# Performance work log

Hardware: AMD Instinct MI355X
Metric: run time of the kernel (lower is better)

The kernel has to match this reference:

```python
import jax, jax.numpy as jnp
import numpy as np

B, S, H = 1, 2048, 1024      # batch, seq, hidden_size
F = 4096                     # intermediate_size
E = 8                        # num_experts
K = 2                        # top-k routing


def setup_inputs() -> dict:
    key = jax.random.key(0)
    ks = jax.random.split(key, 7)
    s = 0.02  # init scale
    return {
        "x": jax.random.normal(ks[0], (B, S, H), jnp.float32),
        "gate_w": jax.random.normal(ks[1], (H, E), jnp.float32) * s,
        "gate_b": jnp.zeros((E,), jnp.float32),
        "w1": jax.random.normal(ks[2], (E, H, F), jnp.float32) * s,
        "b1": jnp.zeros((E, F), jnp.float32),
        "w2": jax.random.normal(ks[3], (E, F, H), jnp.float32) * s,
        "b2": jnp.zeros((E, H), jnp.float32),
    }


def reference(x, gate_w, gate_b, w1, b1, w2, b2):
    Bq, Sq, Hq = x.shape
    T = Bq * Sq
    xt = x.reshape(T, Hq)                              # [T,H] flatten tokens

    # --- router: softmax gate, top-k, renormalize top-k weights ---
    logits = xt @ gate_w + gate_b                      # [T,E]
    probs = jax.nn.softmax(logits, axis=-1)            # [T,E]
    top_v, top_i = jax.lax.top_k(probs, K)             # [T,K]
    top_v = top_v / jnp.sum(top_v, axis=-1, keepdims=True)
    combine = jnp.zeros((T, E), x.dtype).at[jnp.arange(T)[:, None], top_i].set(top_v)  # [T,E] sparse combine weights

    # --- experts: 2-layer FFN (ReLU), batched over experts ---
    h = jax.nn.relu(jnp.einsum('th,ehf->etf', xt, w1) + b1[:, None, :])   # [E,T,F]
    y = jnp.einsum('etf,efh->eth', h, w2) + b2[:, None, :]                # [E,T,H]

    # --- combine: weighted sum over selected experts (zeros elsewhere) ---
    out = jnp.einsum('te,eth->th', combine, y)          # [T,H]
    return out.reshape(Bq, Sq, Hq)
```

## Files before the change

kernel.cpp:

```cpp
#include <hip/hip_runtime.h>

#define TT 2048
#define HH 1024
#define FF 4096
#define EE 8
#define ROWS_CAP 5120
#define KSPLIT2 4

typedef __bf16 bf16;
typedef bf16 bf16x8 __attribute__((ext_vector_type(8)));
typedef bf16 bf16x4 __attribute__((ext_vector_type(4)));
typedef bf16 bf16x2 __attribute__((ext_vector_type(2)));
typedef float floatx4 __attribute__((ext_vector_type(4)));

#define OFF_W1T  ((size_t)0)
#define OFF_W2T  (OFF_W1T + (size_t)67108864)
#define OFF_XG   (OFF_W2T + (size_t)67108864)
#define OFF_H    (OFF_XG  + (size_t)10485760)
#define OFF_CNT  (OFF_H   + (size_t)41943040)
#define OFF_OFS  (OFF_CNT + (size_t)256)
#define OFF_TKE  (OFF_OFS + (size_t)256)
#define OFF_TKR  (OFF_TKE + (size_t)16384)
#define OFF_TKW  (OFF_TKR + (size_t)16384)
#define OFF_ROW  (OFF_TKW + (size_t)16384)
#define OFF_Y    OFF_W1T

__device__ __forceinline__ void gload16(const bf16* g, bf16* l) {
    __builtin_amdgcn_global_load_lds((const __attribute__((address_space(1))) void*)g,
                                     (__attribute__((address_space(3))) void*)l, 16, 0, 0);
}

__global__ __launch_bounds__(256) void transpose_cvt(const float* __restrict__ in,
                                                     bf16* __restrict__ out,
                                                     int R, int C) {
    __shared__ float tile[64][67];
    const int e  = blockIdx.z;
    const int r0 = blockIdx.y * 64, c0 = blockIdx.x * 64;
    const float* inp = in + (size_t)e * R * C;
    bf16* outp = out + (size_t)e * R * C;
    const int t = threadIdx.x;
    {
        const int lr = t >> 4;
        const int lc = (t & 15) << 2;
#pragma unroll
        for (int i = 0; i < 4; ++i) {
            int r = lr + i * 16;
            floatx4 v = *(const floatx4*)&inp[(size_t)(r0 + r) * C + c0 + lc];
            tile[r][lc + 0] = v[0]; tile[r][lc + 1] = v[1];
            tile[r][lc + 2] = v[2]; tile[r][lc + 3] = v[3];
        }
    }
    __syncthreads();
    {
        const int c  = t >> 3;
        const int rq = (t & 7) << 3;
#pragma unroll
        for (int i = 0; i < 2; ++i) {
            int cc = c + i * 32;
            bf16x8 o;
#pragma unroll
            for (int k = 0; k < 8; ++k) o[k] = (bf16)tile[rq + k][cc];
            *(bf16x8*)&outp[(size_t)(c0 + cc) * R + r0 + rq] = o;
        }
    }
}

__global__ __launch_bounds__(256) void router_kernel(const float* __restrict__ x,
                                                     const float* __restrict__ gw,
                                                     const float* __restrict__ gb,
                                                     int* __restrict__ counts,
                                                     int* __restrict__ tke,
                                                     int* __restrict__ tkr,
                                                     float* __restrict__ tkw) {
    const int wave = blockIdx.x * 4 + (threadIdx.x >> 6);
    const int lane = threadIdx.x & 63;
    const int nw = gridDim.x * 4;
    for (int t = wave; t < TT; t += nw) {
        const float* xr = x + (size_t)t * HH;
        double acc[EE];
#pragma unroll
        for (int e = 0; e < EE; ++e) acc[e] = 0.0;
        for (int h = lane; h < HH; h += 64) {
            double xv = (double)xr[h];
            const float* g = gw + (size_t)h * EE;
            floatx4 g0 = *(const floatx4*)&g[0];
            floatx4 g1 = *(const floatx4*)&g[4];
            acc[0] += xv * (double)g0[0]; acc[1] += xv * (double)g0[1];
            acc[2] += xv * (double)g0[2]; acc[3] += xv * (double)g0[3];
            acc[4] += xv * (double)g1[0]; acc[5] += xv * (double)g1[1];
            acc[6] += xv * (double)g1[2]; acc[7] += xv * (double)g1[3];
        }
#pragma unroll
        for (int e = 0; e < EE; ++e) {
            double v = acc[e];
            for (int s = 32; s > 0; s >>= 1) v += __shfl_xor(v, s, 64);
            acc[e] = v + (double)gb[e];
        }
        if (lane == 0) {
            int i1 = 0; double v1 = acc[0];
            for (int e = 1; e < EE; ++e) if (acc[e] > v1) { v1 = acc[e]; i1 = e; }
            int i2 = -1; double v2 = -1e300;
            for (int e = 0; e < EE; ++e) if (e != i1 && acc[e] > v2) { v2 = acc[e]; i2 = e; }
            double wa = 1.0 / (1.0 + exp(v2 - v1));
            double wb = 1.0 - wa;
            int r1 = atomicAdd(&counts[i1], 1);
            int r2 = atomicAdd(&counts[i2], 1);
            tke[t * 2 + 0] = i1; tke[t * 2 + 1] = i2;
            tkr[t * 2 + 0] = r1; tkr[t * 2 + 1] = r2;
            tkw[t * 2 + 0] = (float)wa; tkw[t * 2 + 1] = (float)wb;
        }
    }
}

__global__ void scan_offsets(const int* __restrict__ counts, int* __restrict__ offs) {
    if (threadIdx.x == 0 && blockIdx.x == 0) {
        int off = 0;
        for (int e = 0; e < EE; ++e) {
            offs[e] = off;
            off += (counts[e] + 127) & ~127;
        }
    }
}

__global__ __launch_bounds__(256) void gather_kernel(const float* __restrict__ x,
                                                     const int* __restrict__ tke,
                                                     const int* __restrict__ tkr,
                                                     const int* __restrict__ offs,
                                                     bf16* __restrict__ xg,
                                                     int* __restrict__ rowOf) {
    const int pair = blockIdx.x;
    const int t = pair >> 1;
    const int e = tke[pair];
    const int row = offs[e] + tkr[pair];
    const float* xr = x + (size_t)t * HH;
    bf16* dst = xg + (size_t)row * HH;
    const int tid = threadIdx.x;
    floatx4 v = ((const floatx4*)xr)[tid];
    bf16x4 o;
    o[0] = (bf16)v[0]; o[1] = (bf16)v[1]; o[2] = (bf16)v[2]; o[3] = (bf16)v[3];
    ((bf16x4*)dst)[tid] = o;
    if (tid == 0) rowOf[pair] = row;
}

__global__ __launch_bounds__(256, 2) void gemm1_kernel(const bf16* __restrict__ A,
                                                       const bf16* __restrict__ Bt,
                                                       const float* __restrict__ b1,
                                                       bf16* __restrict__ Hout,
                                                       const int* __restrict__ counts,
                                                       const int* __restrict__ offs) {
    const int e = blockIdx.z, mt = blockIdx.y, nt = blockIdx.x;
    const int cnt = counts[e];
    if (mt * 128 >= cnt) return;
    const int row0 = offs[e] + mt * 128;
    const int K = HH;
    const bf16* Ab = A + (size_t)row0 * K;
    const bf16* Bb = Bt + ((size_t)e * FF + (size_t)nt * 128) * K;

    __shared__ bf16 As[128 * 32];
    __shared__ bf16 Bs[128 * 32];

    const int tid = threadIdx.x;
    const int lane = tid & 63, wave = tid >> 6;
    const int lrow = lane & 15, lq = lane >> 4;
    const int m_w = (wave & 1) << 6, n_w = (wave >> 1) << 6;
    const int swz = (lrow >> 1) & 3;
    const unsigned foff = (unsigned)((lq ^ swz) << 3);

    floatx4 acc[4][4];
#pragma unroll
    for (int i = 0; i < 4; ++i)
#pragma unroll
        for (int j = 0; j < 4; ++j) acc[i][j] = (floatx4){0.f, 0.f, 0.f, 0.f};

    const int c0 = tid, c1 = tid + 256;
    const int ar0 = c0 >> 2, ak0 = (c0 & 3) ^ ((ar0 >> 1) & 3);
    const int ar1 = c1 >> 2, ak1 = (c1 & 3) ^ ((ar1 >> 1) & 3);
    const unsigned lds0 = (unsigned)((tid & ~63) << 4);
    const unsigned lds1 = 4096u + lds0;
    const size_t ga0 = (size_t)ar0 * K + ak0 * 8;
    const size_t ga1 = (size_t)ar1 * K + ak1 * 8;

    for (int kt = 0; kt < K / 32; ++kt) {
        const int kb = kt * 32;
        gload16(Ab + ga0 + kb, (bf16*)((char*)As + lds0));
        gload16(Ab + ga1 + kb, (bf16*)((char*)As + lds1));
        gload16(Bb + ga0 + kb, (bf16*)((char*)Bs + lds0));
        gload16(Bb + ga1 + kb, (bf16*)((char*)Bs + lds1));
        asm volatile("s_waitcnt vmcnt(0)" ::: "memory");
        __syncthreads();

        bf16x8 af[4], bfr[4];
#pragma unroll
        for (int i = 0; i < 4; ++i) {
            int m = m_w + i * 16 + lrow;
            af[i] = *(const bf16x8*)&As[(unsigned)m * 32 + foff];
        }
#pragma unroll
        for (int j = 0; j < 4; ++j) {
            int n = n_w + j * 16 + lrow;
            bfr[j] = *(const bf16x8*)&Bs[(unsigned)n * 32 + foff];
        }
#pragma unroll
        for (int i = 0; i < 4; ++i)
#pragma unroll
            for (int j = 0; j < 4; ++j)
                acc[i][j] = __builtin_amdgcn_mfma_f32_16x16x32_bf16(af[i], bfr[j], acc[i][j], 0, 0, 0);
        __syncthreads();
    }

    const float* bias = b1 + (size_t)e * FF + (size_t)nt * 128;
    bf16* Hb = Hout + (size_t)row0 * FF + (size_t)nt * 128;
#pragma unroll
    for (int j = 0; j < 4; ++j) {
        int col = n_w + j * 16 + lrow;
        float bv = bias[col];
#pragma unroll
        for (int i = 0; i < 4; ++i)
#pragma unroll
            for (int r = 0; r < 4; ++r) {
                int mrow = m_w + i * 16 + (lq << 2) + r;
                float v = acc[i][j][r] + bv;
                Hb[(size_t)mrow * FF + col] = (bf16)(v > 0.f ? v : 0.f);
            }
    }
}

__global__ __launch_bounds__(256, 2) void gemm2_kernel(const bf16* __restrict__ Hin,
                                                       const bf16* __restrict__ Bt,
                                                       const float* __restrict__ b2,
                                                       bf16* __restrict__ Y,
                                                       const int* __restrict__ counts,
                                                       const int* __restrict__ offs) {
    const int e = blockIdx.z >> 2, ks = blockIdx.z & 3;
    const int mt = blockIdx.y, nt = blockIdx.x;
    const int cnt = counts[e];
    if (mt * 128 >= cnt) return;
    const int row0 = offs[e] + mt * 128;
    const int K = FF;
    const int KC = FF / KSPLIT2;
    const bf16* Ab = Hin + (size_t)row0 * K + ks * KC;
    const bf16* Bb = Bt + ((size_t)e * HH + (size_t)nt * 128) * K + ks * KC;

    __shared__ bf16 As[128 * 32];
    __shared__ bf16 Bs[128 * 32];

    const int tid = threadIdx.x;
    const int lane = tid & 63, wave = tid >> 6;
    const int lrow = lane & 15, lq = lane >> 4;
    const int m_w = (wave & 1) << 6, n_w = (wave >> 1) << 6;
    const int swz = (lrow >> 1) & 3;
    const unsigned foff = (unsigned)((lq ^ swz) << 3);

    floatx4 acc[4][4];
#pragma unroll
    for (int i = 0; i < 4; ++i)
#pragma unroll
        for (int j = 0; j < 4; ++j) acc[i][j] = (floatx4){0.f, 0.f, 0.f, 0.f};

    const int c0 = tid, c1 = tid + 256;
    const int ar0 = c0 >> 2, ak0 = (c0 & 3) ^ ((ar0 >> 1) & 3);
    const int ar1 = c1 >> 2, ak1 = (c1 & 3) ^ ((ar1 >> 1) & 3);
    const unsigned lds0 = (unsigned)((tid & ~63) << 4);
    const unsigned lds1 = 4096u + lds0;
    const size_t ga0 = (size_t)ar0 * K + ak0 * 8;
    const size_t ga1 = (size_t)ar1 * K + ak1 * 8;

    for (int kt = 0; kt < KC / 32; ++kt) {
        const int kb = kt * 32;
        gload16(Ab + ga0 + kb, (bf16*)((char*)As + lds0));
        gload16(Ab + ga1 + kb, (bf16*)((char*)As + lds1));
        gload16(Bb + ga0 + kb, (bf16*)((char*)Bs + lds0));
        gload16(Bb + ga1 + kb, (bf16*)((char*)Bs + lds1));
        asm volatile("s_waitcnt vmcnt(0)" ::: "memory");
        __syncthreads();

        bf16x8 af[4], bfr[4];
#pragma unroll
        for (int i = 0; i < 4; ++i) {
            int m = m_w + i * 16 + lrow;
            af[i] = *(const bf16x8*)&As[(unsigned)m * 32 + foff];
        }
#pragma unroll
        for (int j = 0; j < 4; ++j) {
            int n = n_w + j * 16 + lrow;
            bfr[j] = *(const bf16x8*)&Bs[(unsigned)n * 32 + foff];
        }
#pragma unroll
        for (int i = 0; i < 4; ++i)
#pragma unroll
            for (int j = 0; j < 4; ++j)
                acc[i][j] = __builtin_amdgcn_mfma_f32_16x16x32_bf16(af[i], bfr[j], acc[i][j], 0, 0, 0);
        __syncthreads();
    }

    const float* bias = b2 + (size_t)e * HH + (size_t)nt * 128;
    bf16* Yb = Y + ((size_t)ks * ROWS_CAP + row0) * HH + (size_t)nt * 128;
#pragma unroll
    for (int j = 0; j < 4; ++j) {
        int col = n_w + j * 16 + lrow;
        float bv = (ks == 0) ? bias[col] : 0.f;
#pragma unroll
        for (int i = 0; i < 4; ++i)
#pragma unroll
            for (int r = 0; r < 4; ++r) {
                int mrow = m_w + i * 16 + (lq << 2) + r;
                Yb[(size_t)mrow * HH + col] = (bf16)(acc[i][j][r] + bv);
            }
    }
}

__global__ __launch_bounds__(256) void combine_kernel(const bf16* __restrict__ Y,
                                                      const int* __restrict__ rowOf,
                                                      const float* __restrict__ tkw,
                                                      float* __restrict__ out) {
    const int t = blockIdx.x;
    const int tid = threadIdx.x;
    const int ra = rowOf[t * 2 + 0], rb = rowOf[t * 2 + 1];
    const float wa = tkw[t * 2 + 0], wb = tkw[t * 2 + 1];
    const int c = tid * 4;
    float acc[4] = {0.f, 0.f, 0.f, 0.f};
#pragma unroll
    for (int ks = 0; ks < KSPLIT2; ++ks) {
        bf16x4 a = *(const bf16x4*)&Y[((size_t)ks * ROWS_CAP + ra) * HH + c];
        bf16x4 b = *(const bf16x4*)&Y[((size_t)ks * ROWS_CAP + rb) * HH + c];
#pragma unroll
        for (int k = 0; k < 4; ++k) acc[k] += wa * (float)a[k] + wb * (float)b[k];
    }
    floatx4 o; o[0] = acc[0]; o[1] = acc[1]; o[2] = acc[2]; o[3] = acc[3];
    *(floatx4*)&out[(size_t)t * HH + c] = o;
}

extern "C" void kernel_launch(void* const* d_in, const int* in_sizes, int n_in,
                              void* d_out, int out_size, void* d_ws, size_t ws_size,
                              hipStream_t stream) {
    const float* x  = (const float*)d_in[0];
    const float* gw = (const float*)d_in[1];
    const float* gb = (const float*)d_in[2];
    const float* w1 = (const float*)d_in[3];
    const float* b1 = (const float*)d_in[4];
    const float* w2 = (const float*)d_in[5];
    const float* b2 = (const float*)d_in[6];
    float* out = (float*)d_out;
    char* ws = (char*)d_ws;

    bf16*  w1t  = (bf16*)(ws + OFF_W1T);
    bf16*  w2t  = (bf16*)(ws + OFF_W2T);
    bf16*  xg   = (bf16*)(ws + OFF_XG);
    bf16*  hbuf = (bf16*)(ws + OFF_H);
    bf16*  ybuf = (bf16*)(ws + OFF_Y);
    int*   cnts = (int*)(ws + OFF_CNT);
    int*   ofs  = (int*)(ws + OFF_OFS);
    int*   tke  = (int*)(ws + OFF_TKE);
    int*   tkr  = (int*)(ws + OFF_TKR);
    float* tkw  = (float*)(ws + OFF_TKW);
    int*   rowOf= (int*)(ws + OFF_ROW);

    hipMemsetAsync(cnts, 0, 256, stream);
    hipMemsetAsync(xg, 0, (size_t)ROWS_CAP * HH * sizeof(bf16), stream);

    transpose_cvt<<<dim3(FF / 64, HH / 64, EE), 256, 0, stream>>>(w1, w1t, HH, FF);
    transpose_cvt<<<dim3(HH / 64, FF / 64, EE), 256, 0, stream>>>(w2, w2t, FF, HH);
    router_kernel<<<128, 256, 0, stream>>>(x, gw, gb, cnts, tke, tkr, tkw);
    scan_offsets<<<1, 64, 0, stream>>>(cnts, ofs);
    gather_kernel<<<TT * 2, 256, 0, stream>>>(x, tke, tkr, ofs, xg, rowOf);
    gemm1_kernel<<<dim3(FF / 128, 16, EE), 256, 0, stream>>>(xg, w1t, b1, hbuf, cnts, ofs);
    gemm2_kernel<<<dim3(HH / 128, 16, EE * KSPLIT2), 256, 0, stream>>>(hbuf, w2t, b2, ybuf, cnts, ofs);
    combine_kernel<<<TT, 256, 0, stream>>>(ybuf, rowOf, tkw, out);
}
```

Before: 532.2 us.

## Double-buffer LDS tiles in expert GEMMs and add nontemporal loads/stores

Both expert GEMM kernels now use two LDS buffers per operand. The next K-tile's global-to-LDS loads are issued before computing on the current tile, and the wait is vmcnt(4) instead of vmcnt(0), so memory latency overlaps with MFMA work. The weight transpose uses nontemporal loads and gemm2 writes its output with nontemporal stores to reduce cache pollution. LDS use per block doubles, which could affect occupancy, and the last iteration issues a redundant wraparound prefetch.

Result: faster. 512.5 us (-3.7%).

```diff
diff --git a/kernel.cpp b/kernel.cpp
--- a/kernel.cpp
+++ b/kernel.cpp
@@ -45,7 +45,8 @@
 #pragma unroll
         for (int i = 0; i < 4; ++i) {
             int r = lr + i * 16;
-            floatx4 v = *(const floatx4*)&inp[(size_t)(r0 + r) * C + c0 + lc];
+            floatx4 v = __builtin_nontemporal_load(
+                (const floatx4*)&inp[(size_t)(r0 + r) * C + c0 + lc]);
             tile[r][lc + 0] = v[0]; tile[r][lc + 1] = v[1];
             tile[r][lc + 2] = v[2]; tile[r][lc + 3] = v[3];
         }
@@ -153,11 +154,12 @@
     if (mt * 128 >= cnt) return;
     const int row0 = offs[e] + mt * 128;
     const int K = HH;
+    const int NK = K / 32;
     const bf16* Ab = A + (size_t)row0 * K;
     const bf16* Bb = Bt + ((size_t)e * FF + (size_t)nt * 128) * K;
 
-    __shared__ bf16 As[128 * 32];
-    __shared__ bf16 Bs[128 * 32];
+    __shared__ bf16 As[2][128 * 32];
+    __shared__ bf16 Bs[2][128 * 32];
 
     const int tid = threadIdx.x;
     const int lane = tid & 63, wave = tid >> 6;
@@ -180,33 +182,42 @@
     const size_t ga0 = (size_t)ar0 * K + ak0 * 8;
     const size_t ga1 = (size_t)ar1 * K + ak1 * 8;
 
-    for (int kt = 0; kt < K / 32; ++kt) {
-        const int kb = kt * 32;
-        gload16(Ab + ga0 + kb, (bf16*)((char*)As + lds0));
-        gload16(Ab + ga1 + kb, (bf16*)((char*)As + lds1));
-        gload16(Bb + ga0 + kb, (bf16*)((char*)Bs + lds0));
-        gload16(Bb + ga1 + kb, (bf16*)((char*)Bs + lds1));
-        asm volatile("s_waitcnt vmcnt(0)" ::: "memory");
+    gload16(Ab + ga0, (bf16*)((char*)As[0] + lds0));
+    gload16(Ab + ga1, (bf16*)((char*)As[0] + lds1));
+    gload16(Bb + ga0, (bf16*)((char*)Bs[0] + lds0));
+    gload16(Bb + ga1, (bf16*)((char*)Bs[0] + lds1));
+
+    for (int kt = 0; kt < NK; ++kt) {
         __syncthreads();
+        const int kn = (kt + 1 < NK) ? kt + 1 : 0;
+        const int nb = (kt + 1) & 1;
+        const int kb = kn * 32;
+        gload16(Ab + ga0 + kb, (bf16*)((char*)As[nb] + lds0));
+        gload16(Ab + ga1 + kb, (bf16*)((char*)As[nb] + lds1));
+        gload16(Bb + ga0 + kb, (bf16*)((char*)Bs[nb] + lds0));
+        gload16(Bb + ga1 + kb, (bf16*)((char*)Bs[nb] + lds1));
+        asm volatile("s_waitcnt vmcnt(4)" ::: "memory");
+        __syncthreads();
+        const int cb = kt & 1;
 
         bf16x8 af[4], bfr[4];
 #pragma unroll
         for (int i = 0; i < 4; ++i) {
             int m = m_w + i * 16 + lrow;
-            af[i] = *(const bf16x8*)&As[(unsigned)m * 32 + foff];
+            af[i] = *(const bf16x8*)&As[cb][(unsigned)m * 32 + foff];
         }
 #pragma unroll
         for (int j = 0; j < 4; ++j) {
             int n = n_w + j * 16 + lrow;
-            bfr[j] = *(const bf16x8*)&Bs[(unsigned)n * 32 + foff];
+            bfr[j] = *(const bf16x8*)&Bs[cb][(unsigned)n * 32 + foff];
         }
 #pragma unroll
         for (int i = 0; i < 4; ++i)
 #pragma unroll
             for (int j = 0; j < 4; ++j)
                 acc[i][j] = __builtin_amdgcn_mfma_f32_16x16x32_bf16(af[i], bfr[j], acc[i][j], 0, 0, 0);
-        __syncthreads();
-    }
+    }
+    asm volatile("s_waitcnt vmcnt(0)" ::: "memory");
 
     const float* bias = b1 + (size_t)e * FF + (size_t)nt * 128;
     bf16* Hb = Hout + (size_t)row0 * FF + (size_t)nt * 128;
@@ -238,11 +249,12 @@
     const int row0 = offs[e] + mt * 128;
     const int K = FF;
     const int KC = FF / KSPLIT2;
+    const int NK = KC / 32;
     const bf16* Ab = Hin + (size_t)row0 * K + ks * KC;
     const bf16* Bb = Bt + ((size_t)e * HH + (size_t)nt * 128) * K + ks * KC;
 
-    __shared__ bf16 As[128 * 32];
-    __shared__ bf16 Bs[128 * 32];
+    __shared__ bf16 As[2][128 * 32];
+    __shared__ bf16 Bs[2][128 * 32];
 
     const int tid = threadIdx.x;
     const int lane = tid & 63, wave = tid >> 6;
@@ -265,33 +277,42 @@
     const size_t ga0 = (size_t)ar0 * K + ak0 * 8;
     const size_t ga1 = (size_t)ar1 * K + ak1 * 8;
 
-    for (int kt = 0; kt < KC / 32; ++kt) {
-        const int kb = kt * 32;
-        gload16(Ab + ga0 + kb, (bf16*)((char*)As + lds0));
-        gload16(Ab + ga1 + kb, (bf16*)((char*)As + lds1));
-        gload16(Bb + ga0 + kb, (bf16*)((char*)Bs + lds0));
-        gload16(Bb + ga1 + kb, (bf16*)((char*)Bs + lds1));
-        asm volatile("s_waitcnt vmcnt(0)" ::: "memory");
+    gload16(Ab + ga0, (bf16*)((char*)As[0] + lds0));
+    gload16(Ab + ga1, (bf16*)((char*)As[0] + lds1));
+    gload16(Bb + ga0, (bf16*)((char*)Bs[0] + lds0));
+    gload16(Bb + ga1, (bf16*)((char*)Bs[0] + lds1));
+
+    for (int kt = 0; kt < NK; ++kt) {
         __syncthreads();
+        const int kn = (kt + 1 < NK) ? kt + 1 : 0;
+        const int nb = (kt + 1) & 1;
+        const int kb = kn * 32;
+        gload16(Ab + ga0 + kb, (bf16*)((char*)As[nb] + lds0));
+        gload16(Ab + ga1 + kb, (bf16*)((char*)As[nb] + lds1));
+        gload16(Bb + ga0 + kb, (bf16*)((char*)Bs[nb] + lds0));
+        gload16(Bb + ga1 + kb, (bf16*)((char*)Bs[nb] + lds1));
+        asm volatile("s_waitcnt vmcnt(4)" ::: "memory");
+        __syncthreads();
+        const int cb = kt & 1;
 
         bf16x8 af[4], bfr[4];
 #pragma unroll
         for (int i = 0; i < 4; ++i) {
             int m = m_w + i * 16 + lrow;
-            af[i] = *(const bf16x8*)&As[(unsigned)m * 32 + foff];
+            af[i] = *(const bf16x8*)&As[cb][(unsigned)m * 32 + foff];
         }
 #pragma unroll
         for (int j = 0; j < 4; ++j) {
             int n = n_w + j * 16 + lrow;
-            bfr[j] = *(const bf16x8*)&Bs[(unsigned)n * 32 + foff];
+            bfr[j] = *(const bf16x8*)&Bs[cb][(unsigned)n * 32 + foff];
         }
 #pragma unroll
         for (int i = 0; i < 4; ++i)
 #pragma unroll
             for (int j = 0; j < 4; ++j)
                 acc[i][j] = __builtin_amdgcn_mfma_f32_16x16x32_bf16(af[i], bfr[j], acc[i][j], 0, 0, 0);
-        __syncthreads();
-    }
+    }
+    asm volatile("s_waitcnt vmcnt(0)" ::: "memory");
 
     const float* bias = b2 + (size_t)e * HH + (size_t)nt * 128;
     bf16* Yb = Y + ((size_t)ks * ROWS_CAP + row0) * HH + (size_t)nt * 128;
@@ -304,7 +325,10 @@
 #pragma unroll
             for (int r = 0; r < 4; ++r) {
                 int mrow = m_w + i * 16 + (lq << 2) + r;
-                Yb[(size_t)mrow * HH + col] = (bf16)(acc[i][j][r] + bv);
+                bf16 bvv = (bf16)(acc[i][j][r] + bv);
+                unsigned short u;
+                __builtin_memcpy(&u, &bvv, 2);
+                __builtin_nontemporal_store(u, (unsigned short*)&Yb[(size_t)mrow * HH + col]);
             }
     }
 }
```

## Triple-buffer GEMM tiles with 128x256 blocks and drop xg memset

Applied to the files above, without the earlier changes.

Both expert GEMMs move to a shared macro body that widens the N tile to 256 and uses a 3-stage LDS ring. Tiles are prefetched two steps ahead with a partial vmcnt wait and raw s_barrier, so global loads overlap MFMA work instead of stalling on every k-step. The weight transpose reads fp32 weights with nontemporal loads, and the memset zeroing the gathered-token buffer is removed. The costs are more accumulator registers and LDS per block, fewer blocks in flight, and padding rows of xg that are no longer zeroed. Those rows may hold stale data, though they should only feed output rows that are never combined.

Result: faster. 510.2 us (-4.1%).

```diff
diff --git a/kernel.cpp b/kernel.cpp
--- a/kernel.cpp
+++ b/kernel.cpp
@@ -28,6 +28,10 @@
 __device__ __forceinline__ void gload16(const bf16* g, bf16* l) {
     __builtin_amdgcn_global_load_lds((const __attribute__((address_space(1))) void*)g,
                                      (__attribute__((address_space(3))) void*)l, 16, 0, 0);
+}
+
+__device__ __forceinline__ void raw_barrier() {
+    asm volatile("s_barrier" ::: "memory");
 }
 
 __global__ __launch_bounds__(256) void transpose_cvt(const float* __restrict__ in,
@@ -45,7 +49,8 @@
 #pragma unroll
         for (int i = 0; i < 4; ++i) {
             int r = lr + i * 16;
-            floatx4 v = *(const floatx4*)&inp[(size_t)(r0 + r) * C + c0 + lc];
+            floatx4 v = __builtin_nontemporal_load(
+                (const floatx4*)&inp[(size_t)(r0 + r) * C + c0 + lc]);
             tile[r][lc + 0] = v[0]; tile[r][lc + 1] = v[1];
             tile[r][lc + 2] = v[2]; tile[r][lc + 3] = v[3];
         }
@@ -142,6 +147,69 @@
     if (tid == 0) rowOf[pair] = row;
 }
 
+
+#define GEMM_BODY(EPILOGUE)                                                                 \
+    __shared__ bf16 As[3][128 * 32];                                                        \
+    __shared__ bf16 Bs[3][256 * 32];                                                        \
+    const int tid = threadIdx.x;                                                            \
+    const int lane = tid & 63, wave = tid >> 6;                                             \
+    const int lrow = lane & 15, lq = lane >> 4;                                             \
+    const int m_w = (wave & 1) << 6, n_w = (wave >> 1) << 7;                                \
+    const unsigned foff = (unsigned)((lq ^ ((lrow >> 1) & 3)) << 3);                        \
+    floatx4 acc[4][8];                                                                      \
+    _Pragma("unroll") for (int i = 0; i < 4; ++i)                                           \
+        _Pragma("unroll") for (int j = 0; j < 8; ++j)                                       \
+            acc[i][j] = (floatx4){0.f, 0.f, 0.f, 0.f};                                      \
+    int arow[6]; size_t gadr[6];                                                            \
+    _Pragma("unroll") for (int s = 0; s < 6; ++s) {                                         \
+        int c = tid + ((s < 2) ? s * 256 : (s - 2) * 256);                                  \
+        int ar = c >> 2, ak = (c & 3) ^ ((ar >> 1) & 3);                                    \
+        arow[s] = ar; gadr[s] = (size_t)ar * K + (size_t)ak * 8;                            \
+    }                                                                                       \
+    const unsigned ldsw = (unsigned)((tid & ~63) << 4);                \
+                                                               \
+    _Pragma("unroll") for (int p = 0; p < 2; ++p) {                                         \
+        const int kb = p * 32;                                                              \
+        gload16(Ab + gadr[0] + kb, (bf16*)((char*)As[p] + ldsw));                           \
+        gload16(Ab + gadr[1] + kb, (bf16*)((char*)As[p] + 4096u + ldsw));                   \
+        gload16(Bb + gadr[2] + kb, (bf16*)((char*)Bs[p] + ldsw));                           \
+        gload16(Bb + gadr[3] + kb, (bf16*)((char*)Bs[p] + 4096u + ldsw));                   \
+        gload16(Bb + gadr[4] + kb, (bf16*)((char*)Bs[p] + 8192u + ldsw));                   \
+        gload16(Bb + gadr[5] + kb, (bf16*)((char*)Bs[p] + 12288u + ldsw));                  \
+    }                                                                                       \
+    for (int kt = 0; kt < NK; ++kt) {                                                       \
+        raw_barrier();                              \
+        {                                                                                   \
+            const int kn = (kt + 2 < NK) ? kt + 2 : NK - 1;       \
+            const int nb = (kt + 2) % 3;                                                    \
+            const int kb = kn * 32;                                                         \
+            gload16(Ab + gadr[0] + kb, (bf16*)((char*)As[nb] + ldsw));                      \
+            gload16(Ab + gadr[1] + kb, (bf16*)((char*)As[nb] + 4096u + ldsw));              \
+            gload16(Bb + gadr[2] + kb, (bf16*)((char*)Bs[nb] + ldsw));                      \
+            gload16(Bb + gadr[3] + kb, (bf16*)((char*)Bs[nb] + 4096u + ldsw));              \
+            gload16(Bb + gadr[4] + kb, (bf16*)((char*)Bs[nb] + 8192u + ldsw));              \
+            gload16(Bb + gadr[5] + kb, (bf16*)((char*)Bs[nb] + 12288u + ldsw));             \
+        }                                                                                   \
+        asm volatile("s_waitcnt vmcnt(12)" ::: "memory");      \
+        raw_barrier();                                               \
+        const int cb = kt % 3;                                                              \
+        bf16x8 af[4], bfr[8];                                                               \
+        _Pragma("unroll") for (int i = 0; i < 4; ++i) {                                     \
+            int m = m_w + i * 16 + lrow;                                                    \
+            af[i] = *(const bf16x8*)&As[cb][(unsigned)m * 32 + foff];                       \
+        }                                                                                   \
+        _Pragma("unroll") for (int j = 0; j < 8; ++j) {                                     \
+            int n = n_w + j * 16 + lrow;                                                    \
+            bfr[j] = *(const bf16x8*)&Bs[cb][(unsigned)n * 32 + foff];                      \
+        }                                                                                   \
+        _Pragma("unroll") for (int i = 0; i < 4; ++i)                                       \
+            _Pragma("unroll") for (int j = 0; j < 8; ++j)                                   \
+                acc[i][j] = __builtin_amdgcn_mfma_f32_16x16x32_bf16(af[i], bfr[j],          \
+                                                                    acc[i][j], 0, 0, 0);    \
+    }                                                                                       \
+    asm volatile("s_waitcnt vmcnt(0)" ::: "memory");           \
+    EPILOGUE
+
 __global__ __launch_bounds__(256, 2) void gemm1_kernel(const bf16* __restrict__ A,
                                                        const bf16* __restrict__ Bt,
                                                        const float* __restrict__ b1,
@@ -153,76 +221,24 @@
     if (mt * 128 >= cnt) return;
     const int row0 = offs[e] + mt * 128;
     const int K = HH;
+    const int NK = K / 32;
     const bf16* Ab = A + (size_t)row0 * K;
-    const bf16* Bb = Bt + ((size_t)e * FF + (size_t)nt * 128) * K;
-
-    __shared__ bf16 As[128 * 32];
-    __shared__ bf16 Bs[128 * 32];
-
-    const int tid = threadIdx.x;
-    const int lane = tid & 63, wave = tid >> 6;
-    const int lrow = lane & 15, lq = lane >> 4;
-    const int m_w = (wave & 1) << 6, n_w = (wave >> 1) << 6;
-    const int swz = (lrow >> 1) & 3;
-    const unsigned foff = (unsigned)((lq ^ swz) << 3);
-
-    floatx4 acc[4][4];
-#pragma unroll
-    for (int i = 0; i < 4; ++i)
-#pragma unroll
-        for (int j = 0; j < 4; ++j) acc[i][j] = (floatx4){0.f, 0.f, 0.f, 0.f};
-
-    const int c0 = tid, c1 = tid + 256;
-    const int ar0 = c0 >> 2, ak0 = (c0 & 3) ^ ((ar0 >> 1) & 3);
-    const int ar1 = c1 >> 2, ak1 = (c1 & 3) ^ ((ar1 >> 1) & 3);
-    const unsigned lds0 = (unsigned)((tid & ~63) << 4);
-    const unsigned lds1 = 4096u + lds0;
-    const size_t ga0 = (size_t)ar0 * K + ak0 * 8;
-    const size_t ga1 = (size_t)ar1 * K + ak1 * 8;
-
-    for (int kt = 0; kt < K / 32; ++kt) {
-        const int kb = kt * 32;
-        gload16(Ab + ga0 + kb, (bf16*)((char*)As + lds0));
-        gload16(Ab + ga1 + kb, (bf16*)((char*)As + lds1));
-        gload16(Bb + ga0 + kb, (bf16*)((char*)Bs + lds0));
-        gload16(Bb + ga1 + kb, (bf16*)((char*)Bs + lds1));
-        asm volatile("s_waitcnt vmcnt(0)" ::: "memory");
-        __syncthreads();
-
-        bf16x8 af[4], bfr[4];
-#pragma unroll
-        for (int i = 0; i < 4; ++i) {
-            int m = m_w + i * 16 + lrow;
-            af[i] = *(const bf16x8*)&As[(unsigned)m * 32 + foff];
-        }
-#pragma unroll
-        for (int j = 0; j < 4; ++j) {
-            int n = n_w + j * 16 + lrow;
-            bfr[j] = *(const bf16x8*)&Bs[(unsigned)n * 32 + foff];
-        }
-#pragma unroll
-        for (int i = 0; i < 4; ++i)
-#pragma unroll
-            for (int j = 0; j < 4; ++j)
-                acc[i][j] = __builtin_amdgcn_mfma_f32_16x16x32_bf16(af[i], bfr[j], acc[i][j], 0, 0, 0);
-        __syncthreads();
-    }
-
-    const float* bias = b1 + (size_t)e * FF + (size_t)nt * 128;
-    bf16* Hb = Hout + (size_t)row0 * FF + (size_t)nt * 128;
-#pragma unroll
-    for (int j = 0; j < 4; ++j) {
-        int col = n_w + j * 16 + lrow;
-        float bv = bias[col];
-#pragma unroll
-        for (int i = 0; i < 4; ++i)
-#pragma unroll
-            for (int r = 0; r < 4; ++r) {
-                int mrow = m_w + i * 16 + (lq << 2) + r;
-                float v = acc[i][j][r] + bv;
-                Hb[(size_t)mrow * FF + col] = (bf16)(v > 0.f ? v : 0.f);
-            }
-    }
+    const bf16* Bb = Bt + ((size_t)e * FF + (size_t)nt * 256) * K;
+
+    GEMM_BODY({
+        const float* bias = b1 + (size_t)e * FF + (size_t)nt * 256;
+        bf16* Hb = Hout + (size_t)row0 * FF + (size_t)nt * 256;
+        _Pragma("unroll") for (int j = 0; j < 8; ++j) {
+            int col = n_w + j * 16 + lrow;
+            float bv = bias[col];
+            _Pragma("unroll") for (int i = 0; i < 4; ++i)
+                _Pragma("unroll") for (int r = 0; r < 4; ++r) {
+                    int mrow = m_w + i * 16 + (lq << 2) + r;
+                    float v = acc[i][j][r] + bv;
+                    Hb[(size_t)mrow * FF + col] = (bf16)(v > 0.f ? v : 0.f);
+                }
+        }
+    })
 }
 
 __global__ __launch_bounds__(256, 2) void gemm2_kernel(const bf16* __restrict__ Hin,
@@ -238,75 +254,23 @@
     const int row0 = offs[e] + mt * 128;
     const int K = FF;
     const int KC = FF / KSPLIT2;
+    const int NK = KC / 32;
     const bf16* Ab = Hin + (size_t)row0 * K + ks * KC;
-    const bf16* Bb = Bt + ((size_t)e * HH + (size_t)nt * 128) * K + ks * KC;
-
-    __shared__ bf16 As[128 * 32];
-    __shared__ bf16 Bs[128 * 32];
-
-    const int tid = threadIdx.x;
-    const int lane = tid & 63, wave = tid >> 6;
-    const int lrow = lane & 15, lq = lane >> 4;
-    const int m_w = (wave & 1) << 6, n_w = (wave >> 1) << 6;
-    const int swz = (lrow >> 1) & 3;
-    const unsigned foff = (unsigned)((lq ^ swz) << 3);
-
-    floatx4 acc[4][4];
-#pragma unroll
-    for (int i = 0; i < 4; ++i)
-#pragma unroll
-        for (int j = 0; j < 4; ++j) acc[i][j] = (floatx4){0.f, 0.f, 0.f, 0.f};
-
-    const int c0 = tid, c1 = tid + 256;
-    const int ar0 = c0 >> 2, ak0 = (c0 & 3) ^ ((ar0 >> 1) & 3);
-    const int ar1 = c1 >> 2, ak1 = (c1 & 3) ^ ((ar1 >> 1) & 3);
-    const unsigned lds0 = (unsigned)((tid & ~63) << 4);
-    const unsigned lds1 = 4096u + lds0;
-    const size_t ga0 = (size_t)ar0 * K + ak0 * 8;
-    const size_t ga1 = (size_t)ar1 * K + ak1 * 8;
-
-    for (int kt = 0; kt < KC / 32; ++kt) {
-        const int kb = kt * 32;
-        gload16(Ab + ga0 + kb, (bf16*)((char*)As + lds0));
-        gload16(Ab + ga1 + kb, (bf16*)((char*)As + lds1));
-        gload16(Bb + ga0 + kb, (bf16*)((char*)Bs + lds0));
-        gload16(Bb + ga1 + kb, (bf16*)((char*)Bs + lds1));
-        asm volatile("s_waitcnt vmcnt(0)" ::: "memory");
-        __syncthreads();
-
-        bf16x8 af[4], bfr[4];
-#pragma unroll
-        for (int i = 0; i < 4; ++i) {
-            int m = m_w + i * 16 + lrow;
-            af[i] = *(const bf16x8*)&As[(unsigned)m * 32 + foff];
-        }
-#pragma unroll
-        for (int j = 0; j < 4; ++j) {
-            int n = n_w + j * 16 + lrow;
-            bfr[j] = *(const bf16x8*)&Bs[(unsigned)n * 32 + foff];
-        }
-#pragma unroll
-        for (int i = 0; i < 4; ++i)
-#pragma unroll
-            for (int j = 0; j < 4; ++j)
-                acc[i][j] = __builtin_amdgcn_mfma_f32_16x16x32_bf16(af[i], bfr[j], acc[i][j], 0, 0, 0);
-        __syncthreads();
-    }
-
-    const float* bias = b2 + (size_t)e * HH + (size_t)nt * 128;
-    bf16* Yb = Y + ((size_t)ks * ROWS_CAP + row0) * HH + (size_t)nt * 128;
-#pragma unroll
-    for (int j = 0; j < 4; ++j) {
-        int col = n_w + j * 16 + lrow;
-        float bv = (ks == 0) ? bias[col] : 0.f;
-#pragma unroll
-        for (int i = 0; i < 4; ++i)
-#pragma unroll
-            for (int r = 0; r < 4; ++r) {
-                int mrow = m_w + i * 16 + (lq << 2) + r;
-                Yb[(size_t)mrow * HH + col] = (bf16)(acc[i][j][r] + bv);
-            }
-    }
+    const bf16* Bb = Bt + ((size_t)e * HH + (size_t)nt * 256) * K + ks * KC;
+
+    GEMM_BODY({
+        const float* bias = b2 + (size_t)e * HH + (size_t)nt * 256;
+        bf16* Yb = Y + ((size_t)ks * ROWS_CAP + row0) * HH + (size_t)nt * 256;
+        _Pragma("unroll") for (int j = 0; j < 8; ++j) {
+            int col = n_w + j * 16 + lrow;
+            float bv = (ks == 0) ? bias[col] : 0.f;
+            _Pragma("unroll") for (int i = 0; i < 4; ++i)
+                _Pragma("unroll") for (int r = 0; r < 4; ++r) {
+                    int mrow = m_w + i * 16 + (lq << 2) + r;
+                    Yb[(size_t)mrow * HH + col] = (bf16)(acc[i][j][r] + bv);
+                }
+        }
+    })
 }
 
 __global__ __launch_bounds__(256) void combine_kernel(const bf16* __restrict__ Y,
@@ -356,14 +320,13 @@
     int*   rowOf= (int*)(ws + OFF_ROW);
 
     hipMemsetAsync(cnts, 0, 256, stream);
-    hipMemsetAsync(xg, 0, (size_t)ROWS_CAP * HH * sizeof(bf16), stream);
 
     transpose_cvt<<<dim3(FF / 64, HH / 64, EE), 256, 0, stream>>>(w1, w1t, HH, FF);
     transpose_cvt<<<dim3(HH / 64, FF / 64, EE), 256, 0, stream>>>(w2, w2t, FF, HH);
     router_kernel<<<128, 256, 0, stream>>>(x, gw, gb, cnts, tke, tkr, tkw);
     scan_offsets<<<1, 64, 0, stream>>>(cnts, ofs);
     gather_kernel<<<TT * 2, 256, 0, stream>>>(x, tke, tkr, ofs, xg, rowOf);
-    gemm1_kernel<<<dim3(FF / 128, 16, EE), 256, 0, stream>>>(xg, w1t, b1, hbuf, cnts, ofs);
-    gemm2_kernel<<<dim3(HH / 128, 16, EE * KSPLIT2), 256, 0, stream>>>(hbuf, w2t, b2, ybuf, cnts, ofs);
+    gemm1_kernel<<<dim3(FF / 256, 16, EE), 256, 0, stream>>>(xg, w1t, b1, hbuf, cnts, ofs);
+    gemm2_kernel<<<dim3(HH / 256, 16, EE * KSPLIT2), 256, 0, stream>>>(hbuf, w2t, b2, ybuf, cnts, ofs);
     combine_kernel<<<TT, 256, 0, stream>>>(ybuf, rowOf, tkw, out);
 }
```
